# Kernel optimization log

Hardware: AMD Instinct MI355X
Metric: run time of the kernel (lower is better)

## Reference

```python
import jax, jax.numpy as jnp
import numpy as np

B = 4
MAX_N = 2048
D = 512
H = 8
HD = D // H
SRC_LENS = [2048, 1536, 1800, 1200]   # sum = 6584
REF_LENS = [1900, 2048, 1400, 1600]   # sum = 6948
NEG_INF = -1e9


def setup_inputs() -> dict:
    key = jax.random.key(0)
    ks = jax.random.split(key, 8)
    n_src, n_ref = sum(SRC_LENS), sum(REF_LENS)
    s = 0.02
    return {
        "feats_src": jax.random.normal(ks[0], (n_src, D), dtype=jnp.float32),
        "batch_src": jnp.asarray(np.repeat(np.arange(B), SRC_LENS), dtype=jnp.int32),
        "feats_ref": jax.random.normal(ks[1], (n_ref, D), dtype=jnp.float32),
        "batch_ref": jnp.asarray(np.repeat(np.arange(B), REF_LENS), dtype=jnp.int32),
        "w_in": jax.random.normal(ks[2], (3 * D, D), dtype=jnp.float32) * s,
        "b_in": jnp.zeros((3 * D,), dtype=jnp.float32),
        "w_out": jax.random.normal(ks[3], (D, D), dtype=jnp.float32) * s,
        "b_out": jnp.zeros((D,), dtype=jnp.float32),
        "gw1": jax.random.normal(ks[4], (D, D), dtype=jnp.float32) * s,
        "gb1": jnp.zeros((D,), dtype=jnp.float32),
        "gw2": jax.random.normal(ks[5], (1, D), dtype=jnp.float32) * s,
        "gb2": jnp.zeros((1,), dtype=jnp.float32),
    }


def _to_dense(feats, batch_idx):
    # sparse [N, D] (sorted batch indices) -> dense [B, MAX_N, D] + key_padding_mask
    n = feats.shape[0]
    counts = jax.ops.segment_sum(jnp.ones((n,), jnp.int32), batch_idx, num_segments=B)
    starts = jnp.concatenate([jnp.zeros((1,), jnp.int32), jnp.cumsum(counts)[:-1].astype(jnp.int32)])
    pos = jnp.arange(n, dtype=jnp.int32) - starts[batch_idx]  # position within batch
    dense = jnp.zeros((B, MAX_N, feats.shape[1]), feats.dtype).at[batch_idx, pos].set(feats)
    mask = jnp.arange(MAX_N)[None, :] >= counts[:, None]  # True = padding (key_padding_mask)
    return dense, mask, pos


def reference(feats_src, batch_src, feats_ref, batch_ref,
              w_in, b_in, w_out, b_out, gw1, gb1, gw2, gb2):
    d_src, mask_src, pos_src = _to_dense(feats_src, batch_src)
    d_ref, mask_ref, _ = _to_dense(feats_ref, batch_ref)

    # nn.MultiheadAttention (batch_first, eval mode): packed in_proj, scaled dot-product
    q = (d_src @ w_in[:D].T + b_in[:D]).reshape(B, MAX_N, H, HD)
    k = (d_ref @ w_in[D:2 * D].T + b_in[D:2 * D]).reshape(B, MAX_N, H, HD)
    v = (d_ref @ w_in[2 * D:].T + b_in[2 * D:]).reshape(B, MAX_N, H, HD)
    scores = jnp.einsum('bqhd,bkhd->bhqk', q * (HD ** -0.5), k)
    scores = jnp.where(mask_ref[:, None, None, :], NEG_INF, scores)
    attn = jax.nn.softmax(scores, axis=-1)
    ctx = jnp.einsum('bhqk,bkhd->bqhd', attn, v).reshape(B, MAX_N, D)
    d_aligned = ctx @ w_out.T + b_out

    # gate MLP: Linear -> ReLU -> Linear -> Sigmoid
    gate = jax.nn.sigmoid(jax.nn.relu(d_aligned @ gw1.T + gb1) @ gw2.T + gb2)  # [B, MAX_N, 1]
    d_out = d_src + gate * d_aligned

    # dense -> ragged: gather each token back to its flat slot
    out_flat = d_out[batch_src, pos_src]  # [N_src, D]
    return out_flat, gate
```

## Files before the change

### kernel.cpp

```cpp
#include <hip/hip_runtime.h>
#include <hip/hip_bf16.h>


typedef __bf16 bf16x8_t __attribute__((ext_vector_type(8)));
typedef __bf16 bf16x4_t __attribute__((ext_vector_type(4)));
typedef float f32x4_t __attribute__((ext_vector_type(4)));
typedef float f32x2_t __attribute__((ext_vector_type(2)));

#define CQ_SCALE 0.18033688011112042f

__device__ inline bf16x8_t zero8() {
  bf16x8_t z;
#pragma unroll
  for (int t = 0; t < 8; ++t) z[t] = (__bf16)0.0f;
  return z;
}

__device__ __forceinline__ int sniff_f32(const void* w) {
  unsigned short u = ((const unsigned short*)w)[threadIdx.x & 63];
  return __ballot((u & 0x7F80) >= 0x3F80) != 0ULL;
}

__global__ void sentinel_k(float* out) {
  if (threadIdx.x == 0 && blockIdx.x == 0) out[0] = 1000.0f;
}

__global__ void cv_all(const void* w_in, const void* b_in, const void* w_out,
                       const void* b_out, const void* gw1, const void* gb1,
                       const void* gw2, const void* gb2,
                       __hip_bfloat16* __restrict__ ws) {
  int f = sniff_f32(w_in);
  const size_t F_W_IN = 16, F_B_IN = 786448, F_W_OUT = 787984, F_B_OUT = 1050128,
               F_GW1 = 1050640, F_GB1 = 1312784, F_GW2 = 1313296, F_GB2 = 1313808;
  const int total = 1313793;
  for (int g = blockIdx.x * 256 + threadIdx.x; g < total; g += gridDim.x * 256) {
    const void* src;
    size_t dst;
    int i;
    if (g < 786432) { src = w_in; dst = F_W_IN; i = g; }
    else if (g < 787968) { src = b_in; dst = F_B_IN; i = g - 786432; }
    else if (g < 1050112) { src = w_out; dst = F_W_OUT; i = g - 787968; }
    else if (g < 1050624) { src = b_out; dst = F_B_OUT; i = g - 1050112; }
    else if (g < 1312768) { src = gw1; dst = F_GW1; i = g - 1050624; }
    else if (g < 1313280) { src = gb1; dst = F_GB1; i = g - 1312768; }
    else if (g < 1313792) { src = gw2; dst = F_GW2; i = g - 1313280; }
    else { src = gb2; dst = F_GB2; i = g - 1313792; }
    ws[dst + i] = f ? __float2bfloat16(((const float*)src)[i])
                    : ((const __hip_bfloat16*)src)[i];
  }
}

__device__ __forceinline__ void gemm_core(
    const void* __restrict__ A_, long aoff, const __hip_bfloat16* __restrict__ Bt,
    const __hip_bfloat16* __restrict__ bias, __hip_bfloat16* __restrict__ C,
    int M, int K, int lda, int ldc, float cscale, int relu, int f, int bm, int bn,
    __bf16 (&As)[128][64], __bf16 (&Bs)[128][64]) {
  int tid = threadIdx.x, lane = tid & 63, wave = tid >> 6;
  int wm = wave >> 1, wn = wave & 1;
  int l15 = lane & 15, quad = lane >> 4;

  f32x4_t acc[4][4];
#pragma unroll
  for (int i = 0; i < 4; ++i)
#pragma unroll
    for (int j = 0; j < 4; ++j)
#pragma unroll
      for (int r = 0; r < 4; ++r) acc[i][j][r] = 0.f;

  bf16x8_t ra[4], rb[4];
  f32x4_t raf[4][2];

  auto gload = [&](int k0) {
#pragma unroll
    for (int s = 0; s < 4; ++s) {
      int id = s * 256 + tid;
      int row = id >> 3, col = (id & 7) * 8;
      int arow = bm + row;
      if (f) {
        if (arow < M) {
          const float* p = (const float*)A_ + aoff + (size_t)arow * lda + k0 + col;
          raf[s][0] = *reinterpret_cast<const f32x4_t*>(p);
          raf[s][1] = *reinterpret_cast<const f32x4_t*>(p + 4);
        } else {
#pragma unroll
          for (int e = 0; e < 4; ++e) { raf[s][0][e] = 0.f; raf[s][1][e] = 0.f; }
        }
      } else {
        ra[s] = (arow < M)
                    ? *reinterpret_cast<const bf16x8_t*>((const __hip_bfloat16*)A_ + aoff +
                                                         (size_t)arow * lda + k0 + col)
                    : zero8();
      }
      rb[s] = *reinterpret_cast<const bf16x8_t*>(Bt + (size_t)(bn + row) * 512 + k0 + col);
    }
  };
  auto stage = [&]() {
#pragma unroll
    for (int s = 0; s < 4; ++s) {
      int id = s * 256 + tid;
      int row = id >> 3, col = (id & 7) * 8;
      if (f) {
        bf16x8_t t;
#pragma unroll
        for (int e = 0; e < 4; ++e) {
          t[e] = (__bf16)raf[s][0][e];
          t[4 + e] = (__bf16)raf[s][1][e];
        }
        *reinterpret_cast<bf16x8_t*>(&As[row][col]) = t;
      } else {
        *reinterpret_cast<bf16x8_t*>(&As[row][col]) = ra[s];
      }
      *reinterpret_cast<bf16x8_t*>(&Bs[row][col]) = rb[s];
    }
  };

  int nk = K >> 6;
  gload(0);
  for (int it = 0; it < nk; ++it) {
    stage();
    __syncthreads();
    if (it + 1 < nk) gload((it + 1) * 64);
#pragma unroll
    for (int ks = 0; ks < 2; ++ks) {
      bf16x8_t af[4], bfv[4];
#pragma unroll
      for (int i = 0; i < 4; ++i)
        af[i] = *reinterpret_cast<const bf16x8_t*>(
            &As[wm * 64 + i * 16 + l15][ks * 32 + quad * 8]);
#pragma unroll
      for (int j = 0; j < 4; ++j)
        bfv[j] = *reinterpret_cast<const bf16x8_t*>(
            &Bs[wn * 64 + j * 16 + l15][ks * 32 + quad * 8]);
#pragma unroll
      for (int i = 0; i < 4; ++i)
#pragma unroll
        for (int j = 0; j < 4; ++j)
          acc[i][j] = __builtin_amdgcn_mfma_f32_16x16x32_bf16(af[i], bfv[j], acc[i][j], 0, 0, 0);
    }
    __syncthreads();
  }

#pragma unroll
  for (int i = 0; i < 4; ++i)
#pragma unroll
    for (int j = 0; j < 4; ++j) {
      int col = bn + wn * 64 + j * 16 + l15;
      float bv = __bfloat162float(bias[col]);
#pragma unroll
      for (int r = 0; r < 4; ++r) {
        int row = bm + wm * 64 + i * 16 + quad * 4 + r;
        if (row < M) {
          float v = (acc[i][j][r] + bv) * cscale;
          if (relu) v = fmaxf(v, 0.f);
          C[(size_t)row * ldc + col] = __float2bfloat16(v);
        }
      }
    }
}

__global__ __launch_bounds__(256) void proj2(
    const void* __restrict__ fs, const void* __restrict__ fr,
    const __hip_bfloat16* __restrict__ ws, __hip_bfloat16* __restrict__ Q,
    __hip_bfloat16* __restrict__ KV, const void* snf) {
  __shared__ __bf16 As[128][64];
  __shared__ __bf16 Bs[128][64];
  const size_t F_W_IN = 16, F_B_IN = 786448;
  int f = sniff_f32(snf);
  int bid = blockIdx.x;
  if (bid < 208) {
    int bx = bid >> 2, by = bid & 3;
    gemm_core(fs, 0, ws + F_W_IN, ws + F_B_IN, Q, 6584, 512, 512, 512, CQ_SCALE, 0, f,
              bx * 128, by * 128, As, Bs);
  } else {
    int k = bid - 208;
    int bx = k >> 3, by = k & 7;
    gemm_core(fr, 0, ws + F_W_IN + 262144, ws + F_B_IN + 512, KV, 6948, 512, 512, 1024,
              1.0f, 0, f, bx * 128, by * 128, As, Bs);
  }
}

template <bool AF32>
__global__ __launch_bounds__(256) void gemm128(
    const void* __restrict__ A_, long aoff, const __hip_bfloat16* __restrict__ Bt,
    const __hip_bfloat16* __restrict__ bias, __hip_bfloat16* __restrict__ C,
    int M, int K, int lda, int ldc, float cscale, int relu, const void* snf) {
  __shared__ __bf16 As[128][64];
  __shared__ __bf16 Bs[128][64];
  int f = 0;
  if constexpr (AF32) f = sniff_f32(snf);
  gemm_core(A_, aoff, Bt, bias, C, M, K, lda, ldc, cscale, relu, f,
            blockIdx.x * 128, blockIdx.y * 128, As, Bs);
}

template <int NS>
__global__ __launch_bounds__(256) void gemm128_pv(
    const __hip_bfloat16* __restrict__ P, const float* __restrict__ L,
    const __hip_bfloat16* __restrict__ Bt, const __hip_bfloat16* __restrict__ bias,
    __hip_bfloat16* __restrict__ C, int M) {
  const size_t PSZ = 3375104;
  __shared__ __bf16 As[128][64];
  __shared__ __bf16 Bs[128][64];
  int tid = threadIdx.x, lane = tid & 63, wave = tid >> 6;
  int wm = wave >> 1, wn = wave & 1;
  int l15 = lane & 15, quad = lane >> 4;
  int bm = blockIdx.x * 128, bn = blockIdx.y * 128;

  f32x4_t acc[4][4];
#pragma unroll
  for (int i = 0; i < 4; ++i)
#pragma unroll
    for (int j = 0; j < 4; ++j)
#pragma unroll
      for (int r = 0; r < 4; ++r) acc[i][j][r] = 0.f;

  bf16x8_t rp[NS][4], rb[4];
  float rl[4][NS];

  auto gload = [&](int k0) {
    int h = k0 >> 6;
#pragma unroll
    for (int s = 0; s < 4; ++s) {
      int id = s * 256 + tid;
      int row = id >> 3, col = (id & 7) * 8;
      int arow = bm + row;
      if (arow < M) {
        size_t off = (size_t)arow * 512 + k0 + col;
#pragma unroll
        for (int i = 0; i < NS; ++i)
          rp[i][s] = *reinterpret_cast<const bf16x8_t*>(P + i * PSZ + off);
        const float* lp = &L[((size_t)arow * 8 + h) * NS];
#pragma unroll
        for (int i = 0; i < NS; ++i) rl[s][i] = lp[i];
      } else {
#pragma unroll
        for (int i = 0; i < NS; ++i) rp[i][s] = zero8();
        rl[s][0] = 1.f;
#pragma unroll
        for (int i = 1; i < NS; ++i) rl[s][i] = 0.f;
      }
      rb[s] = *reinterpret_cast<const bf16x8_t*>(Bt + (size_t)(bn + row) * 512 + k0 + col);
    }
  };
  auto stage = [&]() {
#pragma unroll
    for (int s = 0; s < 4; ++s) {
      int id = s * 256 + tid;
      int row = id >> 3, col = (id & 7) * 8;
      float sum = 0.f;
#pragma unroll
      for (int i = 0; i < NS; ++i) sum += rl[s][i];
      float sc = 1.0f / sum;
      bf16x8_t t;
#pragma unroll
      for (int e = 0; e < 8; ++e) {
        float v = 0.f;
#pragma unroll
        for (int i = 0; i < NS; ++i) v += rl[s][i] * (float)rp[i][s][e];
        t[e] = (__bf16)(v * sc);
      }
      *reinterpret_cast<bf16x8_t*>(&As[row][col]) = t;
      *reinterpret_cast<bf16x8_t*>(&Bs[row][col]) = rb[s];
    }
  };

  gload(0);
  for (int it = 0; it < 8; ++it) {
    stage();
    __syncthreads();
    if (it + 1 < 8) gload((it + 1) * 64);
#pragma unroll
    for (int ks = 0; ks < 2; ++ks) {
      bf16x8_t af[4], bfv[4];
#pragma unroll
      for (int i = 0; i < 4; ++i)
        af[i] = *reinterpret_cast<const bf16x8_t*>(
            &As[wm * 64 + i * 16 + l15][ks * 32 + quad * 8]);
#pragma unroll
      for (int j = 0; j < 4; ++j)
        bfv[j] = *reinterpret_cast<const bf16x8_t*>(
            &Bs[wn * 64 + j * 16 + l15][ks * 32 + quad * 8]);
#pragma unroll
      for (int i = 0; i < 4; ++i)
#pragma unroll
        for (int j = 0; j < 4; ++j)
          acc[i][j] = __builtin_amdgcn_mfma_f32_16x16x32_bf16(af[i], bfv[j], acc[i][j], 0, 0, 0);
    }
    __syncthreads();
  }

#pragma unroll
  for (int i = 0; i < 4; ++i)
#pragma unroll
    for (int j = 0; j < 4; ++j) {
      int col = bn + wn * 64 + j * 16 + l15;
      float bv = __bfloat162float(bias[col]);
#pragma unroll
      for (int r = 0; r < 4; ++r) {
        int row = bm + wm * 64 + i * 16 + quad * 4 + r;
        if (row < M)
          C[(size_t)row * 512 + col] = __float2bfloat16(acc[i][j][r] + bv);
      }
    }
}

__device__ __forceinline__ void flash_core(
    const __hip_bfloat16* __restrict__ Qb, const __hip_bfloat16* __restrict__ KVb,
    __hip_bfloat16* __restrict__ OUTb, float* __restrict__ LPb, int lns,
    int nsrc, int nref, int qt, int kt0, int ktNfull, int do_tail,
    __bf16 (&VtL)[2][64][72], __bf16 (&PL)[4][32][72]) {
  int h = blockIdx.y;
  int tid = threadIdx.x, lane = tid & 63, wave = tid >> 6;
  int l15 = lane & 15, quad = lane >> 4;
  int Mb = nsrc + 1;
  int qbase = qt * 128 + wave * 32;

  bf16x8_t qfr[2][2];
#pragma unroll
  for (int g = 0; g < 2; ++g) {
    int qrow = qbase + g * 16 + l15;
#pragma unroll
    for (int ks = 0; ks < 2; ++ks)
      qfr[g][ks] = (qrow < nsrc)
                       ? *reinterpret_cast<const bf16x8_t*>(
                             Qb + (size_t)qrow * 512 + h * 64 + ks * 32 + quad * 8)
                       : zero8();
  }

  f32x4_t O[2][4];
#pragma unroll
  for (int g = 0; g < 2; ++g)
#pragma unroll
    for (int j = 0; j < 4; ++j)
#pragma unroll
      for (int r = 0; r < 4; ++r) O[g][j][r] = 0.f;

  f32x4_t Lacc[2];
#pragma unroll
  for (int g = 0; g < 2; ++g)
#pragma unroll
    for (int r = 0; r < 4; ++r) Lacc[g][r] = 0.f;
  bf16x8_t ones;
#pragma unroll
  for (int t = 0; t < 8; ++t) ones[t] = (__bf16)1.0f;

  bf16x8_t kf[8], v0, v1;
  auto loadK = [&](int k0) {
#pragma unroll
    for (int j = 0; j < 4; ++j) {
      const __hip_bfloat16* kp =
          KVb + (size_t)(k0 + j * 16 + l15) * 1024 + h * 64 + quad * 8;
      kf[j * 2] = *reinterpret_cast<const bf16x8_t*>(kp);
      kf[j * 2 + 1] = *reinterpret_cast<const bf16x8_t*>(kp + 32);
    }
  };
  auto loadV = [&](int k0) {
    const __hip_bfloat16* vp = KVb + (size_t)(k0 + lane) * 1024 + 512 + h * 64 + wave * 16;
    v0 = *reinterpret_cast<const bf16x8_t*>(vp);
    v1 = *reinterpret_cast<const bf16x8_t*>(vp + 8);
  };

  int nit = ktNfull - kt0;
  if (nit > 0) {
    loadK(kt0 * 64);
    loadV(kt0 * 64);
  }

  for (int it = 0; it < nit; ++it) {
    int k0 = (kt0 + it) * 64;
    __bf16(*Vt)[72] = VtL[it & 1];
#pragma unroll
    for (int e = 0; e < 8; ++e) {
      Vt[wave * 16 + e][lane] = v0[e];
      Vt[wave * 16 + 8 + e][lane] = v1[e];
    }
    if (it + 1 < nit) loadV(k0 + 64);

#pragma unroll
    for (int g = 0; g < 2; ++g) {
      f32x4_t St[4];
#pragma unroll
      for (int j = 0; j < 4; ++j)
#pragma unroll
        for (int r = 0; r < 4; ++r) St[j][r] = 0.f;
#pragma unroll
      for (int j = 0; j < 4; ++j)
#pragma unroll
        for (int ks = 0; ks < 2; ++ks)
          St[j] = __builtin_amdgcn_mfma_f32_16x16x32_bf16(kf[j * 2 + ks], qfr[g][ks],
                                                          St[j], 0, 0, 0);
#pragma unroll
      for (int j = 0; j < 4; ++j) {
        bf16x4_t pk;
#pragma unroll
        for (int r = 0; r < 4; ++r) pk[r] = (__bf16)exp2f(St[j][r]);
        *reinterpret_cast<bf16x4_t*>(&PL[wave][g * 16 + l15][j * 16 + quad * 4]) = pk;
      }
    }
    if (it + 1 < nit) loadK(k0 + 64);

    __syncthreads();

    bf16x8_t pa[2][2];
#pragma unroll
    for (int g = 0; g < 2; ++g)
#pragma unroll
      for (int ks = 0; ks < 2; ++ks)
        pa[g][ks] = *reinterpret_cast<const bf16x8_t*>(
            &PL[wave][g * 16 + l15][ks * 32 + quad * 8]);
#pragma unroll
    for (int g = 0; g < 2; ++g)
#pragma unroll
      for (int ks = 0; ks < 2; ++ks)
        Lacc[g] = __builtin_amdgcn_mfma_f32_16x16x32_bf16(pa[g][ks], ones, Lacc[g], 0, 0, 0);
#pragma unroll
    for (int j = 0; j < 4; ++j)
#pragma unroll
      for (int ks = 0; ks < 2; ++ks) {
        bf16x8_t vbf =
            *reinterpret_cast<const bf16x8_t*>(&Vt[j * 16 + l15][ks * 32 + quad * 8]);
#pragma unroll
        for (int g = 0; g < 2; ++g)
          O[g][j] = __builtin_amdgcn_mfma_f32_16x16x32_bf16(pa[g][ks], vbf, O[g][j], 0, 0, 0);
      }
  }

  if (do_tail) {
    int k0 = ktNfull * 64;
    __bf16(*Vt)[72] = VtL[nit & 1];
    {
      int kr = k0 + lane;
      const __hip_bfloat16* vp = KVb + (size_t)kr * 1024 + 512 + h * 64 + wave * 16;
      bf16x8_t t0 = (kr < nref) ? *reinterpret_cast<const bf16x8_t*>(vp) : zero8();
      bf16x8_t t1 = (kr < nref) ? *reinterpret_cast<const bf16x8_t*>(vp + 8) : zero8();
#pragma unroll
      for (int e = 0; e < 8; ++e) {
        Vt[wave * 16 + e][lane] = t0[e];
        Vt[wave * 16 + 8 + e][lane] = t1[e];
      }
    }
#pragma unroll
    for (int j = 0; j < 4; ++j) {
      int kcol = k0 + j * 16 + l15;
      const __hip_bfloat16* kp = KVb + (size_t)kcol * 1024 + h * 64 + quad * 8;
      kf[j * 2] = (kcol < nref) ? *reinterpret_cast<const bf16x8_t*>(kp) : zero8();
      kf[j * 2 + 1] = (kcol < nref) ? *reinterpret_cast<const bf16x8_t*>(kp + 32) : zero8();
    }
#pragma unroll
    for (int g = 0; g < 2; ++g) {
      f32x4_t St[4];
#pragma unroll
      for (int j = 0; j < 4; ++j)
#pragma unroll
        for (int r = 0; r < 4; ++r) St[j][r] = 0.f;
#pragma unroll
      for (int j = 0; j < 4; ++j)
#pragma unroll
        for (int ks = 0; ks < 2; ++ks)
          St[j] = __builtin_amdgcn_mfma_f32_16x16x32_bf16(kf[j * 2 + ks], qfr[g][ks],
                                                          St[j], 0, 0, 0);
#pragma unroll
      for (int j = 0; j < 4; ++j) {
        bf16x4_t pk;
#pragma unroll
        for (int r = 0; r < 4; ++r) {
          int kl = k0 + j * 16 + quad * 4 + r;
          pk[r] = (__bf16)((kl < nref) ? exp2f(St[j][r]) : 0.f);
        }
        *reinterpret_cast<bf16x4_t*>(&PL[wave][g * 16 + l15][j * 16 + quad * 4]) = pk;
      }
    }
    __syncthreads();
    bf16x8_t pa[2][2];
#pragma unroll
    for (int g = 0; g < 2; ++g)
#pragma unroll
      for (int ks = 0; ks < 2; ++ks)
        pa[g][ks] = *reinterpret_cast<const bf16x8_t*>(
            &PL[wave][g * 16 + l15][ks * 32 + quad * 8]);
#pragma unroll
    for (int g = 0; g < 2; ++g)
#pragma unroll
      for (int ks = 0; ks < 2; ++ks)
        Lacc[g] = __builtin_amdgcn_mfma_f32_16x16x32_bf16(pa[g][ks], ones, Lacc[g], 0, 0, 0);
#pragma unroll
    for (int j = 0; j < 4; ++j)
#pragma unroll
      for (int ks = 0; ks < 2; ++ks) {
        bf16x8_t vbf =
            *reinterpret_cast<const bf16x8_t*>(&Vt[j * 16 + l15][ks * 32 + quad * 8]);
#pragma unroll
        for (int g = 0; g < 2; ++g)
          O[g][j] = __builtin_amdgcn_mfma_f32_16x16x32_bf16(pa[g][ks], vbf, O[g][j], 0, 0, 0);
      }
  }

  if (LPb && l15 == 0) {
#pragma unroll
    for (int g = 0; g < 2; ++g)
#pragma unroll
      for (int r = 0; r < 4; ++r) {
        int row = qbase + g * 16 + quad * 4 + r;
        if (row < Mb) LPb[((size_t)row * 8 + h) * lns] = Lacc[g][r];
      }
  }

#pragma unroll
  for (int g = 0; g < 2; ++g)
#pragma unroll
    for (int r = 0; r < 4; ++r) {
      int row = qbase + g * 16 + quad * 4 + r;
      if (row < Mb) {
        float inv = 1.0f / Lacc[g][r];
#pragma unroll
        for (int j = 0; j < 4; ++j)
          OUTb[(size_t)row * 512 + h * 64 + j * 16 + l15] =
              __float2bfloat16(O[g][j][r] * inv);
      }
    }
}

__global__ __launch_bounds__(256, 4) void flash_all(
    const __hip_bfloat16* __restrict__ Q, const __hip_bfloat16* __restrict__ KV,
    __hip_bfloat16* __restrict__ P, float* __restrict__ L, int nsplit) {
  const int TILE_START[4] = {0, 17, 30, 45};
  const int SRC_START[4] = {0, 2048, 3584, 5384};
  const int REF_START[4] = {0, 1900, 3948, 5348};
  const int SRC_LEN[4] = {2048, 1536, 1800, 1200};
  const int REF_LEN[4] = {1900, 2048, 1400, 1600};
  const int CS[4] = {0, 2049, 3586, 5387};
  const size_t PSZ = 3375104;
  __shared__ __bf16 VtL[2][64][72];
  __shared__ __bf16 PL[4][32][72];
  int bid = blockIdx.x;
  int b = (bid >= TILE_START[3]) ? 3 : (bid >= TILE_START[2]) ? 2 : (bid >= TILE_START[1]) ? 1 : 0;
  int qt = bid - TILE_START[b];
  int nref = REF_LEN[b];
  int full = nref >> 6, nkt = (nref + 63) >> 6, rem = nref & 63;
  int split = blockIdx.z;
  int kt0 = (nkt * split) / nsplit;
  int ktN, tail;
  if (split == nsplit - 1) { ktN = full; tail = rem > 0; }
  else { ktN = (nkt * (split + 1)) / nsplit; tail = 0; }
  __hip_bfloat16* OUT = P + (size_t)split * PSZ;
  float* LP = (nsplit == 1) ? nullptr : (L + split + (size_t)CS[b] * 8 * nsplit);
  flash_core(Q + (size_t)SRC_START[b] * 512, KV + (size_t)REF_START[b] * 1024,
             OUT + (size_t)CS[b] * 512, LP, nsplit, SRC_LEN[b], nref, qt, kt0, ktN,
             tail, VtL, PL);
}

__global__ __launch_bounds__(256, 4) void flash_one(const __hip_bfloat16* __restrict__ Qb,
                                                    const __hip_bfloat16* __restrict__ KVb,
                                                    __hip_bfloat16* __restrict__ OUTb,
                                                    int nsrc, int nref) {
  __shared__ __bf16 VtL[2][64][72];
  __shared__ __bf16 PL[4][32][72];
  flash_core(Qb, KVb, OUTb, nullptr, 1, nsrc, nref, blockIdx.x, 0, nref >> 6,
             (nref & 63) > 0, VtL, PL);
}

__global__ __launch_bounds__(256) void finalize_all(
    const void* __restrict__ src, const __hip_bfloat16* __restrict__ aligned,
    const __hip_bfloat16* __restrict__ hidden, const __hip_bfloat16* __restrict__ gw2,
    const __hip_bfloat16* __restrict__ gb2, void* __restrict__ out, const void* snf) {
  int f = sniff_f32(snf);
  int lane = threadIdx.x & 63;
  int r = blockIdx.x * 4 + (threadIdx.x >> 6);
  int b = (r >= 5387) ? 3 : (r >= 3586) ? 2 : (r >= 2049) ? 1 : 0;
  const int CS[4] = {0, 2049, 3586, 5387};
  const int NSRC[4] = {2048, 1536, 1800, 1200};
  int pos = r - CS[b];

  float zacc = 0.f;
  const __hip_bfloat16* hrow = hidden + (size_t)r * 512;
#pragma unroll
  for (int t = 0; t < 8; ++t) {
    int c = lane + (t << 6);
    zacc += __bfloat162float(hrow[c]) * __bfloat162float(gw2[c]);
  }
  for (int o = 32; o; o >>= 1) zacc += __shfl_xor(zacc, o);
  zacc += __bfloat162float(gb2[0]);
  float g = 1.f / (1.f + __expf(-zacc));

  const size_t GOFF = (size_t)6584 * 512;
  if (pos < NSRC[b]) {
    size_t ib = (size_t)(r - b) * 512;
    const __hip_bfloat16* arow = aligned + (size_t)r * 512;
#pragma unroll
    for (int t = 0; t < 8; ++t) {
      int c = lane + (t << 6);
      float sv = f ? ((const float*)src)[ib + c]
                   : __bfloat162float(((const __hip_bfloat16*)src)[ib + c]);
      float val = sv + g * __bfloat162float(arow[c]);
      if (f) ((float*)out)[ib + c] = val;
      else ((__hip_bfloat16*)out)[ib + c] = __float2bfloat16(val);
    }
    if (lane == 0) {
      size_t go = GOFF + b * 2048 + pos;
      if (f) ((float*)out)[go] = g;
      else ((__hip_bfloat16*)out)[go] = __float2bfloat16(g);
    }
  } else {
    for (int p = NSRC[b] + lane; p < 2048; p += 64) {
      size_t go = GOFF + b * 2048 + p;
      if (f) ((float*)out)[go] = g;
      else ((__hip_bfloat16*)out)[go] = __float2bfloat16(g);
    }
  }
}

__global__ __launch_bounds__(256) void finalize_b(
    const void* __restrict__ src, const __hip_bfloat16* __restrict__ alnb,
    const __hip_bfloat16* __restrict__ hidb, const __hip_bfloat16* __restrict__ gw2,
    const __hip_bfloat16* __restrict__ gb2, void* __restrict__ out,
    int b, int nsrc, int src_start, const void* snf) {
  int f = sniff_f32(snf);
  int lane = threadIdx.x & 63;
  int r = blockIdx.x * 4 + (threadIdx.x >> 6);
  if (r > nsrc) return;

  float zacc = 0.f;
  const __hip_bfloat16* hrow = hidb + (size_t)r * 512;
#pragma unroll
  for (int t = 0; t < 8; ++t) {
    int c = lane + (t << 6);
    zacc += __bfloat162float(hrow[c]) * __bfloat162float(gw2[c]);
  }
  for (int o = 32; o; o >>= 1) zacc += __shfl_xor(zacc, o);
  zacc += __bfloat162float(gb2[0]);
  float g = 1.f / (1.f + __expf(-zacc));

  const size_t GOFF = (size_t)6584 * 512;
  if (r < nsrc) {
    size_t ib = (size_t)(src_start + r) * 512;
    const __hip_bfloat16* arow = alnb + (size_t)r * 512;
#pragma unroll
    for (int t = 0; t < 8; ++t) {
      int c = lane + (t << 6);
      float sv = f ? ((const float*)src)[ib + c]
                   : __bfloat162float(((const __hip_bfloat16*)src)[ib + c]);
      float val = sv + g * __bfloat162float(arow[c]);
      if (f) ((float*)out)[ib + c] = val;
      else ((__hip_bfloat16*)out)[ib + c] = __float2bfloat16(val);
    }
    if (lane == 0) {
      size_t go = GOFF + b * 2048 + r;
      if (f) ((float*)out)[go] = g;
      else ((__hip_bfloat16*)out)[go] = __float2bfloat16(g);
    }
  } else {
    for (int p = nsrc + lane; p < 2048; p += 64) {
      size_t go = GOFF + b * 2048 + p;
      if (f) ((float*)out)[go] = g;
      else ((__hip_bfloat16*)out)[go] = __float2bfloat16(g);
    }
  }
}

extern "C" void kernel_launch(void* const* d_in, const int* in_sizes, int n_in,
                              void* d_out, int out_size, void* d_ws, size_t ws_size,
                              hipStream_t stream) {
  (void)in_sizes; (void)n_in; (void)out_size;
  const void* feats_src = d_in[0];
  const void* feats_ref = d_in[2];
  const void* w_in = d_in[4];
  const void* b_in = d_in[5];
  const void* w_out = d_in[6];
  const void* b_out = d_in[7];
  const void* gw1 = d_in[8];
  const void* gb1 = d_in[9];
  const void* gw2 = d_in[10];
  const void* gb2 = d_in[11];

  const size_t F_W_IN = 16, F_B_IN = 786448, F_W_OUT = 787984, F_B_OUT = 1050128,
               F_GW1 = 1050640, F_GB1 = 1312784, F_GW2 = 1313296, F_GB2 = 1313808,
               A0 = 1313824;
  const size_t PSZ = 3375104;
  const size_t R3E = A0 + PSZ + 7114752;
  const size_t NEED_A4 = 2 * (R3E + 4 * PSZ + 421632);
  const size_t NEED_A2 = 2 * (R3E + 2 * PSZ + 210816);
  const size_t NEED_A = 2 * (R3E + PSZ);
  const size_t NEED_B = 2 * (A0 + 4259840);

  if (ws_size < NEED_B) {
    sentinel_k<<<1, 64, 0, stream>>>((float*)d_out);
    return;
  }

  __hip_bfloat16* ws = (__hip_bfloat16*)d_ws;
  cv_all<<<dim3(1024), dim3(256), 0, stream>>>(w_in, b_in, w_out, b_out, gw1, gb1, gw2,
                                               gb2, ws);

  const int SRC_LEN[4] = {2048, 1536, 1800, 1200};
  const int REF_LEN[4] = {1900, 2048, 1400, 1600};
  const int SRC_START[4] = {0, 2048, 3584, 5384};
  const int REF_START[4] = {0, 1900, 3948, 5348};
  dim3 blk(256);

  if (ws_size >= NEED_A) {
    __hip_bfloat16* R1 = ws + A0;
    __hip_bfloat16* R2 = R1 + PSZ;
    __hip_bfloat16* R3 = R2 + 7114752;
    proj2<<<dim3(648), blk, 0, stream>>>(feats_src, feats_ref, ws, R1, R2, w_in);
    int NS = (ws_size >= NEED_A4) ? 4 : (ws_size >= NEED_A2) ? 2 : 1;
    if (NS >= 2) {
      float* L = (float*)(ws + R3E + (size_t)NS * PSZ);
      flash_all<<<dim3(55, 8, NS), blk, 0, stream>>>(R1, R2, R3, L, NS);
      if (NS == 4)
        gemm128_pv<4><<<dim3(52, 4), blk, 0, stream>>>(R3, L, ws + F_W_OUT,
                                                       ws + F_B_OUT, R1, 6588);
      else
        gemm128_pv<2><<<dim3(52, 4), blk, 0, stream>>>(R3, L, ws + F_W_OUT,
                                                       ws + F_B_OUT, R1, 6588);
    } else {
      flash_all<<<dim3(55, 8, 1), blk, 0, stream>>>(R1, R2, R3, nullptr, 1);
      gemm128<false><<<dim3(52, 4), blk, 0, stream>>>(R3, 0, ws + F_W_OUT, ws + F_B_OUT,
                                                      R1, 6588, 512, 512, 512, 1.0f, 0,
                                                      nullptr);
    }
    gemm128<false><<<dim3(52, 4), blk, 0, stream>>>(R1, 0, ws + F_GW1, ws + F_GB1, R3,
                                                    6588, 512, 512, 512, 1.0f, 1,
                                                    nullptr);
    finalize_all<<<dim3(1647), blk, 0, stream>>>(feats_src, R1, R3, ws + F_GW2,
                                                 ws + F_GB2, d_out, w_in);
  } else {
    __hip_bfloat16* W2 = ws + A0;
    __hip_bfloat16* W1 = W2 + 2097152;
    __hip_bfloat16* W3 = W1 + 1081344;
    for (int b = 0; b < 4; ++b) {
      int nsrc = SRC_LEN[b], nref = REF_LEN[b];
      gemm128<true><<<dim3((nsrc + 127) / 128, 4), blk, 0, stream>>>(
          feats_src, (long)SRC_START[b] * 512, ws + F_W_IN, ws + F_B_IN, W1, nsrc, 512,
          512, 512, CQ_SCALE, 0, w_in);
      gemm128<true><<<dim3((nref + 127) / 128, 8), blk, 0, stream>>>(
          feats_ref, (long)REF_START[b] * 512, ws + F_W_IN + 262144, ws + F_B_IN + 512,
          W2, nref, 512, 512, 1024, 1.0f, 0, w_in);
      flash_one<<<dim3((nsrc + 128) / 128, 8), blk, 0, stream>>>(W1, W2, W3, nsrc, nref);
      gemm128<false><<<dim3((nsrc + 128) / 128, 4), blk, 0, stream>>>(
          W3, 0, ws + F_W_OUT, ws + F_B_OUT, W1, nsrc + 1, 512, 512, 512, 1.0f, 0,
          nullptr);
      gemm128<false><<<dim3((nsrc + 128) / 128, 4), blk, 0, stream>>>(
          W1, 0, ws + F_GW1, ws + F_GB1, W3, nsrc + 1, 512, 512, 512, 1.0f, 1, nullptr);
      finalize_b<<<dim3((nsrc + 4) / 4), blk, 0, stream>>>(
          feats_src, W1, W3, ws + F_GW2, ws + F_GB2, d_out, b, nsrc, SRC_START[b], w_in);
    }
  }
}
```

Baseline: 268.4 us.

## Store K/V in head-major contiguous layout and cap flash split at two

The K/V projection epilogue now writes each 64-column head chunk into its own contiguous [rows x 64] slab instead of an interleaved 1024-wide row layout. The flash kernels read K and V from these per-head slabs, so each K/V tile is a dense contiguous block rather than 128-byte pieces strided 2 KB apart. The 4-way KV split path is also removed, so the split count is at most two, which reduces partial-output traffic and the cost of the later merge but leaves fewer blocks to fill the GPU. The GEMM epilogue's writes become scattered across slabs.

```diff
diff --git a/kernel.cpp b/kernel.cpp
--- a/kernel.cpp
+++ b/kernel.cpp
@@ -54,7 +54,7 @@
     const void* __restrict__ A_, long aoff, const __hip_bfloat16* __restrict__ Bt,
     const __hip_bfloat16* __restrict__ bias, __hip_bfloat16* __restrict__ C,
     int M, int K, int lda, int ldc, float cscale, int relu, int f, int bm, int bn,
-    __bf16 (&As)[128][64], __bf16 (&Bs)[128][64]) {
+    long chs, __bf16 (&As)[128][64], __bf16 (&Bs)[128][64]) {
   int tid = threadIdx.x, lane = tid & 63, wave = tid >> 6;
   int wm = wave >> 1, wn = wave & 1;
   int l15 = lane & 15, quad = lane >> 4;
@@ -152,7 +152,9 @@
         if (row < M) {
           float v = (acc[i][j][r] + bv) * cscale;
           if (relu) v = fmaxf(v, 0.f);
-          C[(size_t)row * ldc + col] = __float2bfloat16(v);
+          size_t idx = chs ? ((size_t)(col >> 6) * chs + (size_t)row * 64 + (col & 63))
+                           : ((size_t)row * ldc + col);
+          C[idx] = __float2bfloat16(v);
         }
       }
     }
@@ -165,17 +167,18 @@
   __shared__ __bf16 As[128][64];
   __shared__ __bf16 Bs[128][64];
   const size_t F_W_IN = 16, F_B_IN = 786448;
+  const long CHS = (long)6948 * 64;
   int f = sniff_f32(snf);
   int bid = blockIdx.x;
   if (bid < 208) {
     int bx = bid >> 2, by = bid & 3;
     gemm_core(fs, 0, ws + F_W_IN, ws + F_B_IN, Q, 6584, 512, 512, 512, CQ_SCALE, 0, f,
-              bx * 128, by * 128, As, Bs);
+              bx * 128, by * 128, 0, As, Bs);
   } else {
     int k = bid - 208;
     int bx = k >> 3, by = k & 7;
     gemm_core(fr, 0, ws + F_W_IN + 262144, ws + F_B_IN + 512, KV, 6948, 512, 512, 1024,
-              1.0f, 0, f, bx * 128, by * 128, As, Bs);
+              1.0f, 0, f, bx * 128, by * 128, CHS, As, Bs);
   }
 }
 
@@ -183,13 +186,14 @@
 __global__ __launch_bounds__(256) void gemm128(
     const void* __restrict__ A_, long aoff, const __hip_bfloat16* __restrict__ Bt,
     const __hip_bfloat16* __restrict__ bias, __hip_bfloat16* __restrict__ C,
-    int M, int K, int lda, int ldc, float cscale, int relu, const void* snf) {
+    int M, int K, int lda, int ldc, float cscale, int relu, long chs,
+    const void* snf) {
   __shared__ __bf16 As[128][64];
   __shared__ __bf16 Bs[128][64];
   int f = 0;
   if constexpr (AF32) f = sniff_f32(snf);
   gemm_core(A_, aoff, Bt, bias, C, M, K, lda, ldc, cscale, relu, f,
-            blockIdx.x * 128, blockIdx.y * 128, As, Bs);
+            blockIdx.x * 128, blockIdx.y * 128, chs, As, Bs);
 }
 
 template <int NS>
@@ -304,10 +308,10 @@
 }
 
 __device__ __forceinline__ void flash_core(
-    const __hip_bfloat16* __restrict__ Qb, const __hip_bfloat16* __restrict__ KVb,
-    __hip_bfloat16* __restrict__ OUTb, float* __restrict__ LPb, int lns,
-    int nsrc, int nref, int qt, int kt0, int ktNfull, int do_tail,
-    __bf16 (&VtL)[2][64][72], __bf16 (&PL)[4][32][72]) {
+    const __hip_bfloat16* __restrict__ Qb, const __hip_bfloat16* __restrict__ Kb,
+    const __hip_bfloat16* __restrict__ Vb, __hip_bfloat16* __restrict__ OUTb,
+    float* __restrict__ LPb, int lns, int nsrc, int nref, int qt, int kt0,
+    int ktNfull, int do_tail, __bf16 (&VtL)[2][64][72], __bf16 (&PL)[4][32][72]) {
   int h = blockIdx.y;
   int tid = threadIdx.x, lane = tid & 63, wave = tid >> 6;
   int l15 = lane & 15, quad = lane >> 4;
@@ -347,14 +351,13 @@
   auto loadK = [&](int k0) {
 #pragma unroll
     for (int j = 0; j < 4; ++j) {
-      const __hip_bfloat16* kp =
-          KVb + (size_t)(k0 + j * 16 + l15) * 1024 + h * 64 + quad * 8;
+      const __hip_bfloat16* kp = Kb + (size_t)(k0 + j * 16 + l15) * 64 + quad * 8;
       kf[j * 2] = *reinterpret_cast<const bf16x8_t*>(kp);
       kf[j * 2 + 1] = *reinterpret_cast<const bf16x8_t*>(kp + 32);
     }
   };
   auto loadV = [&](int k0) {
-    const __hip_bfloat16* vp = KVb + (size_t)(k0 + lane) * 1024 + 512 + h * 64 + wave * 16;
+    const __hip_bfloat16* vp = Vb + (size_t)(k0 + lane) * 64 + wave * 16;
     v0 = *reinterpret_cast<const bf16x8_t*>(vp);
     v1 = *reinterpret_cast<const bf16x8_t*>(vp + 8);
   };
@@ -429,7 +432,7 @@
     __bf16(*Vt)[72] = VtL[nit & 1];
     {
       int kr = k0 + lane;
-      const __hip_bfloat16* vp = KVb + (size_t)kr * 1024 + 512 + h * 64 + wave * 16;
+      const __hip_bfloat16* vp = Vb + (size_t)kr * 64 + wave * 16;
       bf16x8_t t0 = (kr < nref) ? *reinterpret_cast<const bf16x8_t*>(vp) : zero8();
       bf16x8_t t1 = (kr < nref) ? *reinterpret_cast<const bf16x8_t*>(vp + 8) : zero8();
 #pragma unroll
@@ -441,7 +444,7 @@
 #pragma unroll
     for (int j = 0; j < 4; ++j) {
       int kcol = k0 + j * 16 + l15;
-      const __hip_bfloat16* kp = KVb + (size_t)kcol * 1024 + h * 64 + quad * 8;
+      const __hip_bfloat16* kp = Kb + (size_t)kcol * 64 + quad * 8;
       kf[j * 2] = (kcol < nref) ? *reinterpret_cast<const bf16x8_t*>(kp) : zero8();
       kf[j * 2 + 1] = (kcol < nref) ? *reinterpret_cast<const bf16x8_t*>(kp + 32) : zero8();
     }
@@ -529,6 +532,7 @@
   const int REF_LEN[4] = {1900, 2048, 1400, 1600};
   const int CS[4] = {0, 2049, 3586, 5387};
   const size_t PSZ = 3375104;
+  const size_t CHS = (size_t)6948 * 64;
   __shared__ __bf16 VtL[2][64][72];
   __shared__ __bf16 PL[4][32][72];
   int bid = blockIdx.x;
@@ -541,20 +545,25 @@
   int ktN, tail;
   if (split == nsplit - 1) { ktN = full; tail = rem > 0; }
   else { ktN = (nkt * (split + 1)) / nsplit; tail = 0; }
+  int h = blockIdx.y;
+  const __hip_bfloat16* Kb = KV + (size_t)h * CHS + (size_t)REF_START[b] * 64;
+  const __hip_bfloat16* Vb = KV + (size_t)(8 + h) * CHS + (size_t)REF_START[b] * 64;
   __hip_bfloat16* OUT = P + (size_t)split * PSZ;
   float* LP = (nsplit == 1) ? nullptr : (L + split + (size_t)CS[b] * 8 * nsplit);
-  flash_core(Q + (size_t)SRC_START[b] * 512, KV + (size_t)REF_START[b] * 1024,
-             OUT + (size_t)CS[b] * 512, LP, nsplit, SRC_LEN[b], nref, qt, kt0, ktN,
-             tail, VtL, PL);
+  flash_core(Q + (size_t)SRC_START[b] * 512, Kb, Vb, OUT + (size_t)CS[b] * 512, LP,
+             nsplit, SRC_LEN[b], nref, qt, kt0, ktN, tail, VtL, PL);
 }
 
 __global__ __launch_bounds__(256, 4) void flash_one(const __hip_bfloat16* __restrict__ Qb,
                                                     const __hip_bfloat16* __restrict__ KVb,
                                                     __hip_bfloat16* __restrict__ OUTb,
-                                                    int nsrc, int nref) {
+                                                    int nsrc, int nref, long chs) {
   __shared__ __bf16 VtL[2][64][72];
   __shared__ __bf16 PL[4][32][72];
-  flash_core(Qb, KVb, OUTb, nullptr, 1, nsrc, nref, blockIdx.x, 0, nref >> 6,
+  int h = blockIdx.y;
+  const __hip_bfloat16* Kb = KVb + (size_t)h * chs;
+  const __hip_bfloat16* Vb = KVb + (size_t)(8 + h) * chs;
+  flash_core(Qb, Kb, Vb, OUTb, nullptr, 1, nsrc, nref, blockIdx.x, 0, nref >> 6,
              (nref & 63) > 0, VtL, PL);
 }
 
@@ -676,7 +685,6 @@
                A0 = 1313824;
   const size_t PSZ = 3375104;
   const size_t R3E = A0 + PSZ + 7114752;
-  const size_t NEED_A4 = 2 * (R3E + 4 * PSZ + 421632);
   const size_t NEED_A2 = 2 * (R3E + 2 * PSZ + 210816);
   const size_t NEED_A = 2 * (R3E + PSZ);
   const size_t NEED_B = 2 * (A0 + 4259840);
@@ -701,24 +709,20 @@
     __hip_bfloat16* R2 = R1 + PSZ;
     __hip_bfloat16* R3 = R2 + 7114752;
     proj2<<<dim3(648), blk, 0, stream>>>(feats_src, feats_ref, ws, R1, R2, w_in);
-    int NS = (ws_size >= NEED_A4) ? 4 : (ws_size >= NEED_A2) ? 2 : 1;
-    if (NS >= 2) {
-      float* L = (float*)(ws + R3E + (size_t)NS * PSZ);
-      flash_all<<<dim3(55, 8, NS), blk, 0, stream>>>(R1, R2, R3, L, NS);
-      if (NS == 4)
-        gemm128_pv<4><<<dim3(52, 4), blk, 0, stream>>>(R3, L, ws + F_W_OUT,
-                                                       ws + F_B_OUT, R1, 6588);
-      else
-        gemm128_pv<2><<<dim3(52, 4), blk, 0, stream>>>(R3, L, ws + F_W_OUT,
-                                                       ws + F_B_OUT, R1, 6588);
+    int NS = (ws_size >= NEED_A2) ? 2 : 1;
+    if (NS == 2) {
+      float* L = (float*)(ws + R3E + 2 * PSZ);
+      flash_all<<<dim3(55, 8, 2), blk, 0, stream>>>(R1, R2, R3, L, 2);
+      gemm128_pv<2><<<dim3(52, 4), blk, 0, stream>>>(R3, L, ws + F_W_OUT,
+                                                     ws + F_B_OUT, R1, 6588);
     } else {
       flash_all<<<dim3(55, 8, 1), blk, 0, stream>>>(R1, R2, R3, nullptr, 1);
       gemm128<false><<<dim3(52, 4), blk, 0, stream>>>(R3, 0, ws + F_W_OUT, ws + F_B_OUT,
                                                       R1, 6588, 512, 512, 512, 1.0f, 0,
-                                                      nullptr);
+                                                      0, nullptr);
     }
     gemm128<false><<<dim3(52, 4), blk, 0, stream>>>(R1, 0, ws + F_GW1, ws + F_GB1, R3,
-                                                    6588, 512, 512, 512, 1.0f, 1,
+                                                    6588, 512, 512, 512, 1.0f, 1, 0,
                                                     nullptr);
     finalize_all<<<dim3(1647), blk, 0, stream>>>(feats_src, R1, R3, ws + F_GW2,
                                                  ws + F_GB2, d_out, w_in);
@@ -726,20 +730,23 @@
     __hip_bfloat16* W2 = ws + A0;
     __hip_bfloat16* W1 = W2 + 2097152;
     __hip_bfloat16* W3 = W1 + 1081344;
+    const long CHS_B = (long)2048 * 64;
     for (int b = 0; b < 4; ++b) {
       int nsrc = SRC_LEN[b], nref = REF_LEN[b];
       gemm128<true><<<dim3((nsrc + 127) / 128, 4), blk, 0, stream>>>(
           feats_src, (long)SRC_START[b] * 512, ws + F_W_IN, ws + F_B_IN, W1, nsrc, 512,
-          512, 512, CQ_SCALE, 0, w_in);
+          512, 512, CQ_SCALE, 0, 0, w_in);
       gemm128<true><<<dim3((nref + 127) / 128, 8), blk, 0, stream>>>(
           feats_ref, (long)REF_START[b] * 512, ws + F_W_IN + 262144, ws + F_B_IN + 512,
-          W2, nref, 512, 512, 1024, 1.0f, 0, w_in);
-      flash_one<<<dim3((nsrc + 128) / 128, 8), blk, 0, stream>>>(W1, W2, W3, nsrc, nref);
+          W2, nref, 512, 512, 1024, 1.0f, 0, CHS_B, w_in);
+      flash_one<<<dim3((nsrc + 128) / 128, 8), blk, 0, stream>>>(W1, W2, W3, nsrc, nref,
+                                                                 CHS_B);
       gemm128<false><<<dim3((nsrc + 128) / 128, 4), blk, 0, stream>>>(
-          W3, 0, ws + F_W_OUT, ws + F_B_OUT, W1, nsrc + 1, 512, 512, 512, 1.0f, 0,
+          W3, 0, ws + F_W_OUT, ws + F_B_OUT, W1, nsrc + 1, 512, 512, 512, 1.0f, 0, 0,
           nullptr);
       gemm128<false><<<dim3((nsrc + 128) / 128, 4), blk, 0, stream>>>(
-          W1, 0, ws + F_GW1, ws + F_GB1, W3, nsrc + 1, 512, 512, 512, 1.0f, 1, nullptr);
+          W1, 0, ws + F_GW1, ws + F_GB1, W3, nsrc + 1, 512, 512, 512, 1.0f, 1, 0,
+          nullptr);
       finalize_b<<<dim3((nsrc + 4) / 4), blk, 0, stream>>>(
           feats_src, W1, W3, ws + F_GW2, ws + F_GB2, d_out, b, nsrc, SRC_START[b], w_in);
     }
```

Result: no change. 264.8 us (-1.4%).
